# Kernel tuning notes

Hardware: AMD Instinct MI355X
Metric: run time of the kernel (lower is better)

Reference implementation:

```python
import jax, jax.numpy as jnp
import numpy as np


def _gelu(x):
    # torch F.gelu default = exact (erf) gelu
    return jax.nn.gelu(x, approximate=False)


def _gatv2(x, src, dst, Wl, bl, Wr, br, att, bout, n):
    """PyG GATv2Conv, concat=False (mean over heads), negative_slope=0.2."""
    H, C = att.shape
    xl = (x @ Wl + bl).reshape(n, H, C)  # source-side transform (messages)
    xr = (x @ Wr + br).reshape(n, H, C)  # target-side transform
    e = jax.nn.leaky_relu(xl[src] + xr[dst], 0.2)      # [E,H,C]
    logits = jnp.einsum('ehc,hc->eh', e, att)          # [E,H]
    # segment softmax over incoming edges of each target node
    m = jax.ops.segment_max(logits, dst, num_segments=n)
    m = jnp.where(jnp.isfinite(m), m, 0.0)
    p = jnp.exp(logits - m[dst])
    den = jax.ops.segment_sum(p, dst, num_segments=n)
    alpha = p / (den[dst] + 1e-16)
    out = jax.ops.segment_sum(alpha[:, :, None] * xl[src], dst, num_segments=n)  # [N,H,C]
    return out.mean(axis=1) + bout


def _gnorm(x, w, b, ms):
    """PyG GraphNorm with a single graph (batch == zeros)."""
    mu = x.mean(axis=0, keepdims=True)
    o = x - ms * mu
    var = (o * o).mean(axis=0, keepdims=True)
    return w * o / jnp.sqrt(var + 1e-5) + b


def setup_inputs() -> dict:
    N, E, HID, LAT = 50000, 300000, 128, 256
    key = jax.random.key(0)
    ks = iter(jax.random.split(key, 48))

    def rn(shape, s=0.05):
        return jax.random.normal(next(ks), shape, jnp.float32) * s

    d = {}
    d['z_g'] = rn((1, LAT), 1.0)
    d['edge_index'] = jax.random.randint(next(ks), (2, E), 0, N, dtype=jnp.int32)
    d['template_vertices'] = rn((N, 3), 1.0)
    d['W_ne1'] = rn((3, HID)); d['b_ne1'] = jnp.zeros((HID,))
    d['W_ne2'] = rn((HID, HID)); d['b_ne2'] = jnp.zeros((HID,))
    d['W_s1'] = rn((LAT, HID)); d['b_s1'] = jnp.zeros((HID,))
    d['W_s2'] = rn((HID, HID)); d['b_s2'] = jnp.zeros((HID,))
    for i, h in ((1, 2), (2, 2), (3, 1)):
        d[f'Wl{i}'] = rn((HID, h * HID)); d[f'bl{i}'] = jnp.zeros((h * HID,))
        d[f'Wr{i}'] = rn((HID, h * HID)); d[f'br{i}'] = jnp.zeros((h * HID,))
        d[f'att{i}'] = rn((h, HID)); d[f'bo{i}'] = jnp.zeros((HID,))
        d[f'gn{i}_w'] = jnp.ones((HID,)); d[f'gn{i}_b'] = jnp.zeros((HID,))
        d[f'gn{i}_ms'] = jnp.ones((HID,))
    d['W_h1'] = rn((HID, HID // 2)); d['b_h1'] = jnp.zeros((HID // 2,))
    d['W_h2'] = rn((HID // 2, 3)); d['b_h2'] = jnp.zeros((3,))
    return d


def reference(z_g, edge_index, template_vertices,
              W_ne1, b_ne1, W_ne2, b_ne2, W_s1, b_s1, W_s2, b_s2,
              Wl1, bl1, Wr1, br1, att1, bo1, gn1_w, gn1_b, gn1_ms,
              Wl2, bl2, Wr2, br2, att2, bo2, gn2_w, gn2_b, gn2_ms,
              Wl3, bl3, Wr3, br3, att3, bo3, gn3_w, gn3_b, gn3_ms,
              W_h1, b_h1, W_h2, b_h2):
    n = template_vertices.shape[0]
    sl = jnp.arange(n, dtype=edge_index.dtype)
    src = jnp.concatenate([edge_index[0], sl])  # GATv2Conv add_self_loops=True
    dst = jnp.concatenate([edge_index[1], sl])
    # node embedding + broadcast style (eval mode -> dropout is identity)
    x = _gelu(template_vertices @ W_ne1 + b_ne1) @ W_ne2 + b_ne2
    style = _gelu(z_g @ W_s1 + b_s1) @ W_s2 + b_s2   # [1, hidden]
    x = x + style
    x = _gelu(_gnorm(_gatv2(x, src, dst, Wl1, bl1, Wr1, br1, att1, bo1, n), gn1_w, gn1_b, gn1_ms))
    x = _gelu(_gnorm(_gatv2(x, src, dst, Wl2, bl2, Wr2, br2, att2, bo2, n), gn2_w, gn2_b, gn2_ms))
    x = _gelu(_gnorm(_gatv2(x, src, dst, Wl3, bl3, Wr3, br3, att3, bo3, n), gn3_w, gn3_b, gn3_ms))
    displacement = _gelu(x @ W_h1 + b_h1) @ W_h2 + b_h2   # [n, 3]
    return displacement
```

## Files before the change

### kernel.cpp

```cpp
#include <hip/hip_runtime.h>
#include <hip/hip_fp16.h>
#include <math.h>

#define DEVINL __device__ __forceinline__

using bf16x8 = __attribute__((ext_vector_type(8))) short;
using f32x4  = __attribute__((ext_vector_type(4))) float;
using u16x4  = __attribute__((ext_vector_type(4))) unsigned short;
using f16x2  = __attribute__((ext_vector_type(2))) _Float16;

DEVINL float gelu_f(float v) { return 0.5f * v * (1.0f + erff(v * 0.7071067811865475f)); }
DEVINL float lrelu_f(float v) { return v > 0.0f ? v : 0.2f * v; }
DEVINL unsigned short f2bf(float f) {
    union { float f; unsigned u; } c; c.f = f;
    unsigned r = c.u + 0x7fffu + ((c.u >> 16) & 1u);
    return (unsigned short)(r >> 16);
}
DEVINL float bf2f(unsigned short s) {
    union { unsigned u; float f; } c; c.u = (unsigned)s << 16;
    return c.f;
}
DEVINL unsigned short f2h(float f) {
    __half h = __float2half_rn(f);
    return *(unsigned short*)&h;
}
DEVINL f16x2 b2h2(unsigned u) {
    union { unsigned u; f16x2 h; } c; c.u = u; return c.h;
}
DEVINL void gl_lds16(const void* g, void* l) {
    __builtin_amdgcn_global_load_lds(
        (const __attribute__((address_space(1))) unsigned*)g,
        (__attribute__((address_space(3))) unsigned*)l, 16, 0, 0);
}

__global__ void style_k(const float* __restrict__ zg, const float* __restrict__ W1,
                        const float* __restrict__ b1, const float* __restrict__ W2,
                        const float* __restrict__ b2, float* __restrict__ style) {
    __shared__ float s1[128];
    int j = threadIdx.x;
    float a = b1[j];
    for (int k = 0; k < 256; k++) a = fmaf(zg[k], W1[k * 128 + j], a);
    s1[j] = gelu_f(a);
    __syncthreads();
    float o = b2[j];
    for (int k = 0; k < 128; k++) o = fmaf(s1[k], W2[k * 128 + j], o);
    style[j] = o;
}

__global__ void ne1_k(const float* __restrict__ tv, const float* __restrict__ W,
                      const float* __restrict__ b, float* __restrict__ h1,
                      int* __restrict__ counts, int Nn) {
    int idx = blockIdx.x * blockDim.x + threadIdx.x;
    if (idx < Nn) counts[idx] = 0;
    if (idx >= Nn * 128) return;
    int n = idx >> 7, c = idx & 127;
    float o = fmaf(tv[n * 3 + 0], W[c],
              fmaf(tv[n * 3 + 1], W[128 + c],
              fmaf(tv[n * 3 + 2], W[256 + c], b[c])));
    h1[idx] = gelu_f(o);
}

struct PrepArgs {
    const float* src[8];
    unsigned short* dst;
    int dstoff[8];
    int off[9];
    int shift[8];
};
__global__ void prep_k(PrepArgs a) {
    int idx = blockIdx.x * 256 + threadIdx.x;
    if (idx >= a.off[8]) return;
    int s = 0;
    while (idx >= a.off[s + 1]) s++;
    int e = idx - a.off[s];
    int sh = a.shift[s];
    int k = e >> sh, j = e & ((1 << sh) - 1);
    float w = a.src[s][e];
    unsigned short hi = f2bf(w);
    unsigned short lo = f2bf(w - bf2f(hi));
    int c = j >> 4, lr = j & 15;
    int s2 = k >> 5, lk = (k >> 3) & 3, i = k & 7;
    int lane = lk * 16 + lr;
    size_t base = (size_t)a.dstoff[s] + (size_t)c * 4096 + s2 * 512 + lane * 8 + i;
    a.dst[base] = hi;
    a.dst[base + 2048] = lo;
}

template <int OUT, int EPI, bool DUAL, typename OutT>
__global__ __launch_bounds__(256) void mfma_lin_k(
    const float* __restrict__ xin,
    const unsigned short* __restrict__ WT0, const float* __restrict__ b0,
    const unsigned short* __restrict__ WT1, const float* __restrict__ b1,
    const float* __restrict__ style,
    OutT* __restrict__ out0, OutT* __restrict__ out1, int Nn) {
    constexpr int CPM = OUT / 16;
    constexpr int NCH = (DUAL ? 2 : 1) * CPM;
    __shared__ uint4 buf[2][512];
    int t = threadIdx.x;
    int wave = t >> 6, lane = t & 63;
    int lr = lane & 15, lk = lane >> 4;
    int base = blockIdx.x * 128 + wave * 32;
    int r0 = base + lr, r1 = base + 16 + lr;
    int cr0 = min(r0, Nn - 1), cr1 = min(r1, Nn - 1);

    bf16x8 xh[2][4], xlo[2][4];
#pragma unroll
    for (int rr = 0; rr < 2; rr++) {
        const float* px = xin + (size_t)(rr ? cr1 : cr0) * 128;
#pragma unroll
        for (int s = 0; s < 4; s++) {
            const float4* p4 = (const float4*)(px + s * 32 + lk * 8);
            float4 a = p4[0], b = p4[1];
            float v[8] = {a.x, a.y, a.z, a.w, b.x, b.y, b.z, b.w};
            bf16x8 h, l;
#pragma unroll
            for (int i = 0; i < 8; i++) {
                unsigned short hb = f2bf(v[i]);
                h[i] = (short)hb;
                l[i] = (short)f2bf(v[i] - bf2f(hb));
            }
            xh[rr][s] = h;
            xlo[rr][s] = l;
        }
    }

    auto stage = [&](int c, int bsel) {
        const unsigned short* Wt = (DUAL && c >= CPM) ? WT1 : WT0;
        int cc = (DUAL && c >= CPM) ? c - CPM : c;
        const char* g = (const char*)(Wt + (size_t)cc * 4096);
        char* l = (char*)&buf[bsel][0];
        gl_lds16(g + t * 16, l + wave * 1024);
        gl_lds16(g + 4096 + t * 16, l + 4096 + wave * 1024);
    };

    stage(0, 0);
    for (int c = 0; c < NCH; ++c) {
        int cur = c & 1;
        bool pre = (c + 1 < NCH);
        if (pre) stage(c + 1, cur ^ 1);
        if (pre) asm volatile("s_waitcnt vmcnt(2)" ::: "memory");
        else     asm volatile("s_waitcnt vmcnt(0)" ::: "memory");
        __builtin_amdgcn_s_barrier();

        int m = (DUAL && c >= CPM) ? 1 : 0;
        int j0 = (c - m * CPM) * 16;
        const float* bias = m ? b1 : b0;
        OutT* out = m ? out1 : out0;
        const bf16x8* W = (const bf16x8*)&buf[cur][0];

        f32x4 acc0 = {0.f, 0.f, 0.f, 0.f}, acc1 = {0.f, 0.f, 0.f, 0.f};
#pragma unroll
        for (int s = 0; s < 4; ++s) {
            bf16x8 wh = W[s * 64 + lane];
            bf16x8 wl = W[256 + s * 64 + lane];
            acc0 = __builtin_amdgcn_mfma_f32_16x16x32_bf16(wh, xh[0][s], acc0, 0, 0, 0);
            acc0 = __builtin_amdgcn_mfma_f32_16x16x32_bf16(wh, xlo[0][s], acc0, 0, 0, 0);
            acc0 = __builtin_amdgcn_mfma_f32_16x16x32_bf16(wl, xh[0][s], acc0, 0, 0, 0);
            acc1 = __builtin_amdgcn_mfma_f32_16x16x32_bf16(wh, xh[1][s], acc1, 0, 0, 0);
            acc1 = __builtin_amdgcn_mfma_f32_16x16x32_bf16(wh, xlo[1][s], acc1, 0, 0, 0);
            acc1 = __builtin_amdgcn_mfma_f32_16x16x32_bf16(wl, xh[1][s], acc1, 0, 0, 0);
        }
        int j = j0 + lk * 4;
        float o0[4], o1[4];
#pragma unroll
        for (int i = 0; i < 4; i++) {
            float bb = bias[j + i];
            if (EPI == 1) bb += style[j + i];
            float v0 = acc0[i] + bb, v1 = acc1[i] + bb;
            if (EPI == 2) { v0 = gelu_f(v0); v1 = gelu_f(v1); }
            o0[i] = v0; o1[i] = v1;
        }
        if constexpr (sizeof(OutT) == 2) {
            u16x4 s0 = {f2h(o0[0]), f2h(o0[1]), f2h(o0[2]), f2h(o0[3])};
            u16x4 s1v = {f2h(o1[0]), f2h(o1[1]), f2h(o1[2]), f2h(o1[3])};
            if (r0 < Nn) *(u16x4*)((unsigned short*)out + (size_t)r0 * OUT + j) = s0;
            if (r1 < Nn) *(u16x4*)((unsigned short*)out + (size_t)r1 * OUT + j) = s1v;
        } else {
            if (r0 < Nn) { f32x4 v = {o0[0], o0[1], o0[2], o0[3]}; *(f32x4*)((float*)out + (size_t)r0 * OUT + j) = v; }
            if (r1 < Nn) { f32x4 v = {o1[0], o1[1], o1[2], o1[3]}; *(f32x4*)((float*)out + (size_t)r1 * OUT + j) = v; }
        }
        __builtin_amdgcn_s_barrier();
    }
}

__global__ void count_k(const int* __restrict__ dst, int* __restrict__ counts, int E, int EP) {
    int e = blockIdx.x * blockDim.x + threadIdx.x;
    if (e >= EP) return;
    int d = (e < E) ? dst[e] : (e - E);
    atomicAdd(&counts[d], 1);
}

__global__ void tile_sum_k(const int* __restrict__ counts, int* __restrict__ tsum, int Nn) {
    int i = blockIdx.x * 256 + threadIdx.x;
    int v = (i < Nn) ? counts[i] : 0;
    int lane = threadIdx.x & 63, wave = threadIdx.x >> 6;
#pragma unroll
    for (int off = 1; off < 64; off <<= 1) v += __shfl_xor(v, off, 64);
    __shared__ int red[4];
    if (lane == 0) red[wave] = v;
    __syncthreads();
    if (threadIdx.x == 0) tsum[blockIdx.x] = red[0] + red[1] + red[2] + red[3];
}

__global__ void tile_scan_k(const int* __restrict__ tsum, int* __restrict__ toff,
                            int ntiles, int* __restrict__ rowptr, int Nn, int total) {
    __shared__ int s[256];
    int t = threadIdx.x;
    int v = (t < ntiles) ? tsum[t] : 0;
    s[t] = v;
    __syncthreads();
    for (int off = 1; off < 256; off <<= 1) {
        int a = (t >= off) ? s[t - off] : 0;
        __syncthreads();
        s[t] += a;
        __syncthreads();
    }
    if (t < ntiles) toff[t] = s[t] - v;
    if (t == 0) rowptr[Nn] = total;
}

__global__ void tile_write_k(const int* __restrict__ counts, const int* __restrict__ toff,
                             int* __restrict__ rowptr, int* __restrict__ fillc, int Nn) {
    int i = blockIdx.x * 256 + threadIdx.x;
    int t = threadIdx.x;
    int v = (i < Nn) ? counts[i] : 0;
    if (i < Nn) fillc[i] = 0;
    __shared__ int s[256];
    s[t] = v;
    __syncthreads();
    for (int off = 1; off < 256; off <<= 1) {
        int a = (t >= off) ? s[t - off] : 0;
        __syncthreads();
        s[t] += a;
        __syncthreads();
    }
    if (i < Nn) rowptr[i] = toff[blockIdx.x] + s[t] - v;
}

__global__ void fill_k(const int* __restrict__ src, const int* __restrict__ dst,
                       const int* __restrict__ rowptr, int* __restrict__ fillc,
                       int* __restrict__ col, int E, int EP) {
    int e = blockIdx.x * blockDim.x + threadIdx.x;
    if (e >= EP) return;
    int d = (e < E) ? dst[e] : (e - E);
    int s = (e < E) ? src[e] : (e - E);
    int pos = atomicAdd(&fillc[d], 1);
    col[rowptr[d] + pos] = s;
}

template <int H>
__global__ __launch_bounds__(256) void gat_gather_k(
    const unsigned short* __restrict__ xl, const unsigned short* __restrict__ xr,
    const float* __restrict__ att, const float* __restrict__ bo,
    const int* __restrict__ rowptr, const int* __restrict__ col,
    float* __restrict__ y, float* __restrict__ stats, int Nn) {
    if (blockIdx.x == 0 && threadIdx.x < 256) stats[threadIdx.x] = 0.f;
    constexpr int NPB = (H == 2) ? 2 : 4;
    int w = threadIdx.x >> 6;
    int slot = (H == 2) ? (w >> 1) : w;
    int h = (H == 2) ? (w & 1) : 0;
    int lane = threadIdx.x & 63;
    int g = lane >> 4, sub = lane & 15;
    constexpr int HC = H * 128;
    int n = blockIdx.x * NPB + slot;
    bool act = n < Nn;
    int nn = act ? n : 0;

    uint4 uxr = *(const uint4*)(xr + (size_t)nn * HC + h * 128 + sub * 8);
    f16x2 xrv[4] = {b2h2(uxr.x), b2h2(uxr.y), b2h2(uxr.z), b2h2(uxr.w)};
    const float* ap = att + h * 128 + sub * 8;
    f16x2 a2[4];
#pragma unroll
    for (int i = 0; i < 4; i++) {
        f16x2 t; t.x = (_Float16)ap[2 * i]; t.y = (_Float16)ap[2 * i + 1];
        a2[i] = t;
    }
    f16x2 c02; c02.x = (_Float16)0.2f; c02.y = (_Float16)0.2f;

    float den = 0.f;
    float acc[8] = {0.f, 0.f, 0.f, 0.f, 0.f, 0.f, 0.f, 0.f};
    int beg = act ? rowptr[n] : 0, endp = act ? rowptr[n + 1] : 0;

    for (int k0 = beg; k0 < endp; k0 += 4) {
        int k = k0 + g;
        bool ev = k < endp;
        int s = col[ev ? k : beg];
        uint4 u = *(const uint4*)(xl + (size_t)s * HC + h * 128 + sub * 8);
        f16x2 v2[4] = {b2h2(u.x), b2h2(u.y), b2h2(u.z), b2h2(u.w)};
        float p = 0.f;
#pragma unroll
        for (int i = 0; i < 4; i++) {
            f16x2 t = v2[i] + xrv[i];
            f16x2 e = __builtin_elementwise_max(t, t * c02);
#if __has_builtin(__builtin_amdgcn_fdot2)
            p = __builtin_amdgcn_fdot2(e, a2[i], p, false);
#else
            p = fmaf((float)e.x, (float)a2[i].x, p);
            p = fmaf((float)e.y, (float)a2[i].y, p);
#endif
        }
        p += __shfl_xor(p, 1, 64);
        p += __shfl_xor(p, 2, 64);
        p += __shfl_xor(p, 4, 64);
        p += __shfl_xor(p, 8, 64);
        float pe = ev ? __expf(p) : 0.f;
        den += pe;
#pragma unroll
        for (int i = 0; i < 4; i++) {
            acc[2 * i]     = fmaf(pe, (float)v2[i].x, acc[2 * i]);
            acc[2 * i + 1] = fmaf(pe, (float)v2[i].y, acc[2 * i + 1]);
        }
    }
#pragma unroll
    for (int off = 16; off <= 32; off <<= 1) {
        den += __shfl_xor(den, off, 64);
#pragma unroll
        for (int j = 0; j < 8; j++) acc[j] += __shfl_xor(acc[j], off, 64);
    }
    float inv = 1.0f / (den + 1e-16f);

    if constexpr (H == 1) {
        if (act && g == 0) {
            const float* bp = bo + sub * 8;
            f32x4 o0 = {acc[0] * inv + bp[0], acc[1] * inv + bp[1], acc[2] * inv + bp[2], acc[3] * inv + bp[3]};
            f32x4 o1 = {acc[4] * inv + bp[4], acc[5] * inv + bp[5], acc[6] * inv + bp[6], acc[7] * inv + bp[7]};
            *(f32x4*)(y + (size_t)n * 128 + sub * 8) = o0;
            *(f32x4*)(y + (size_t)n * 128 + sub * 8 + 4) = o1;
        }
    } else {
        __shared__ float sh[NPB][2][128];
        if (g == 0) {
#pragma unroll
            for (int j = 0; j < 8; j++) sh[slot][h][sub * 8 + j] = acc[j] * inv;
        }
        __syncthreads();
        int t = threadIdx.x;
        int slot2 = t >> 7, c = t & 127;
        int n2 = blockIdx.x * NPB + slot2;
        if (n2 < Nn)
            y[(size_t)n2 * 128 + c] = (sh[slot2][0][c] + sh[slot2][1][c]) * 0.5f + bo[c];
    }
}

__global__ void gn_stats_k(const float* __restrict__ y, float* __restrict__ stats, int Nn) {
    int c = threadIdx.x;
    int per = (Nn + gridDim.x - 1) / gridDim.x;
    int n0 = blockIdx.x * per, n1 = min(n0 + per, Nn);
    float s = 0.f, s2 = 0.f;
    for (int n = n0; n < n1; n++) {
        float v = y[(size_t)n * 128 + c];
        s += v;
        s2 = fmaf(v, v, s2);
    }
    atomicAdd(&stats[c], s);
    atomicAdd(&stats[128 + c], s2);
}

__global__ void gn_apply_k(const float* __restrict__ y, const float* __restrict__ stats,
                           const float* __restrict__ w, const float* __restrict__ b,
                           const float* __restrict__ ms, float* __restrict__ xo, int Nn) {
    int i4 = blockIdx.x * blockDim.x + threadIdx.x;
    if (i4 >= Nn * 32) return;
    float4 v = reinterpret_cast<const float4*>(y)[i4];
    int c0 = (i4 & 31) * 4;
    float o[4] = {v.x, v.y, v.z, v.w};
    float invN = 1.0f / (float)Nn;
#pragma unroll
    for (int jj = 0; jj < 4; jj++) {
        int c = c0 + jj;
        float mu = stats[c] * invN;
        float ex2 = stats[128 + c] * invN;
        float msv = ms[c];
        float var = ex2 - 2.f * msv * mu * mu + msv * msv * mu * mu;
        float ov = o[jj] - msv * mu;
        float r = rsqrtf(var + 1e-5f);
        o[jj] = gelu_f(fmaf(w[c], ov * r, b[c]));
    }
    float4 res = make_float4(o[0], o[1], o[2], o[3]);
    reinterpret_cast<float4*>(xo)[i4] = res;
}

__global__ void head2_k(const float* __restrict__ h, const float* __restrict__ W,
                        const float* __restrict__ b, float* __restrict__ out, int Nn) {
    __shared__ float w[192];
    __shared__ float bb[3];
    int t = threadIdx.x;
    if (t < 192) w[t] = W[t];
    if (t < 3) bb[t] = b[t];
    __syncthreads();
    int n = blockIdx.x * blockDim.x + t;
    if (n >= Nn) return;
    float a0 = bb[0], a1 = bb[1], a2 = bb[2];
    const float4* h4 = reinterpret_cast<const float4*>(h + (size_t)n * 64);
    for (int k4 = 0; k4 < 16; k4++) {
        float4 v = h4[k4];
        int k = k4 * 4;
        a0 = fmaf(v.x, w[(k + 0) * 3 + 0], a0); a1 = fmaf(v.x, w[(k + 0) * 3 + 1], a1); a2 = fmaf(v.x, w[(k + 0) * 3 + 2], a2);
        a0 = fmaf(v.y, w[(k + 1) * 3 + 0], a0); a1 = fmaf(v.y, w[(k + 1) * 3 + 1], a1); a2 = fmaf(v.y, w[(k + 1) * 3 + 2], a2);
        a0 = fmaf(v.z, w[(k + 2) * 3 + 0], a0); a1 = fmaf(v.z, w[(k + 2) * 3 + 1], a1); a2 = fmaf(v.z, w[(k + 2) * 3 + 2], a2);
        a0 = fmaf(v.w, w[(k + 3) * 3 + 0], a0); a1 = fmaf(v.w, w[(k + 3) * 3 + 1], a1); a2 = fmaf(v.w, w[(k + 3) * 3 + 2], a2);
    }
    out[n * 3 + 0] = a0;
    out[n * 3 + 1] = a1;
    out[n * 3 + 2] = a2;
}

extern "C" void kernel_launch(void* const* d_in, const int* in_sizes, int n_in,
                              void* d_out, int out_size, void* d_ws, size_t ws_size,
                              hipStream_t stream) {
    const float* zg = (const float*)d_in[0];
    const int* ei = (const int*)d_in[1];
    const float* tv = (const float*)d_in[2];
    const float* W_ne1 = (const float*)d_in[3];
    const float* b_ne1 = (const float*)d_in[4];
    const float* W_ne2 = (const float*)d_in[5];
    const float* b_ne2 = (const float*)d_in[6];
    const float* W_s1 = (const float*)d_in[7];
    const float* b_s1 = (const float*)d_in[8];
    const float* W_s2 = (const float*)d_in[9];
    const float* b_s2 = (const float*)d_in[10];
    const float *Wl[3], *bl[3], *Wr[3], *br[3], *attp[3], *bop[3], *gnw[3], *gnb[3], *gnms[3];
    for (int L = 0; L < 3; L++) {
        int base = 11 + L * 9;
        Wl[L] = (const float*)d_in[base + 0];
        bl[L] = (const float*)d_in[base + 1];
        Wr[L] = (const float*)d_in[base + 2];
        br[L] = (const float*)d_in[base + 3];
        attp[L] = (const float*)d_in[base + 4];
        bop[L] = (const float*)d_in[base + 5];
        gnw[L] = (const float*)d_in[base + 6];
        gnb[L] = (const float*)d_in[base + 7];
        gnms[L] = (const float*)d_in[base + 8];
    }
    const float* W_h1 = (const float*)d_in[38];
    const float* b_h1 = (const float*)d_in[39];
    const float* W_h2 = (const float*)d_in[40];
    const float* b_h2 = (const float*)d_in[41];

    int E = in_sizes[1] / 2;
    int N = in_sizes[2] / 3;
    int EP = E + N;
    int NT = (N + 255) / 256;
    const int* srcp = ei;
    const int* dstp = ei + E;

    char* p = (char*)d_ws;
    auto alloc = [&](size_t bytes) -> char* {
        char* r = p;
        p += (bytes + 255) & ~(size_t)255;
        return r;
    };
    float* style = (float*)alloc(512);
    float* h1 = (float*)alloc((size_t)N * 128 * 4);
    float* x = (float*)alloc((size_t)N * 128 * 4);
    unsigned short* xle = (unsigned short*)alloc((size_t)N * 256 * 2);
    unsigned short* xre = (unsigned short*)alloc((size_t)N * 256 * 2);
    float* y = (float*)alloc((size_t)N * 128 * 4);
    float* hb = (float*)alloc((size_t)N * 64 * 4);
    float* stats = (float*)alloc(1024);
    int* rowptr = (int*)alloc(((size_t)N + 1) * 4);
    int* counts = (int*)alloc((size_t)N * 4);
    int* fillc = (int*)alloc((size_t)N * 4);
    int* col = (int*)alloc((size_t)EP * 4);
    int* tsum = (int*)alloc((size_t)NT * 4);
    int* toff = (int*)alloc((size_t)NT * 4);
    unsigned short* wt = (unsigned short*)alloc((size_t)376832 * 2);

    PrepArgs pa;
    const float* srcs[8] = {W_ne2, Wl[0], Wr[0], Wl[1], Wr[1], Wl[2], Wr[2], W_h1};
    int outs[8] = {128, 256, 256, 256, 256, 128, 128, 64};
    int off = 0;
    pa.dst = wt;
    for (int s = 0; s < 8; s++) {
        pa.src[s] = srcs[s];
        pa.off[s] = off;
        pa.dstoff[s] = 2 * off;
        pa.shift[s] = (outs[s] == 256) ? 8 : (outs[s] == 128 ? 7 : 6);
        off += 128 * outs[s];
    }
    pa.off[8] = off;
    const unsigned short* ws_ne2 = wt + pa.dstoff[0];
    const unsigned short* ws_l[3] = {wt + pa.dstoff[1], wt + pa.dstoff[3], wt + pa.dstoff[5]};
    const unsigned short* ws_r[3] = {wt + pa.dstoff[2], wt + pa.dstoff[4], wt + pa.dstoff[6]};
    const unsigned short* ws_h1 = wt + pa.dstoff[7];
    prep_k<<<(off + 255) / 256, 256, 0, stream>>>(pa);

    style_k<<<1, 128, 0, stream>>>(zg, W_s1, b_s1, W_s2, b_s2, style);
    ne1_k<<<(N * 128 + 255) / 256, 256, 0, stream>>>(tv, W_ne1, b_ne1, h1, counts, N);
    mfma_lin_k<128, 1, false, float><<<(N + 127) / 128, 256, 0, stream>>>(
        h1, ws_ne2, b_ne2, nullptr, nullptr, style, x, nullptr, N);

    count_k<<<(EP + 255) / 256, 256, 0, stream>>>(dstp, counts, E, EP);
    tile_sum_k<<<NT, 256, 0, stream>>>(counts, tsum, N);
    tile_scan_k<<<1, 256, 0, stream>>>(tsum, toff, NT, rowptr, N, EP);
    tile_write_k<<<NT, 256, 0, stream>>>(counts, toff, rowptr, fillc, N);
    fill_k<<<(EP + 255) / 256, 256, 0, stream>>>(srcp, dstp, rowptr, fillc, col, E, EP);

    const int HS[3] = {2, 2, 1};
    for (int L = 0; L < 3; L++) {
        if (HS[L] == 2) {
            mfma_lin_k<256, 0, true, unsigned short><<<(N + 127) / 128, 256, 0, stream>>>(
                x, ws_l[L], bl[L], ws_r[L], br[L], nullptr, xle, xre, N);
            gat_gather_k<2><<<(N + 1) / 2, 256, 0, stream>>>(xle, xre, attp[L], bop[L], rowptr, col, y, stats, N);
        } else {
            mfma_lin_k<128, 0, true, unsigned short><<<(N + 127) / 128, 256, 0, stream>>>(
                x, ws_l[L], bl[L], ws_r[L], br[L], nullptr, xle, xre, N);
            gat_gather_k<1><<<(N + 3) / 4, 256, 0, stream>>>(xle, xre, attp[L], bop[L], rowptr, col, y, stats, N);
        }
        gn_stats_k<<<512, 128, 0, stream>>>(y, stats, N);
        gn_apply_k<<<(N * 32 + 255) / 256, 256, 0, stream>>>(y, stats, gnw[L], gnb[L], gnms[L], x, N);
    }

    mfma_lin_k<64, 2, false, float><<<(N + 127) / 128, 256, 0, stream>>>(
        x, ws_h1, b_h1, nullptr, nullptr, nullptr, hb, nullptr, N);
    head2_k<<<(N + 255) / 256, 256, 0, stream>>>(hb, W_h2, b_h2, (float*)d_out, N);
}
```

Baseline: 667.0 us.

## Fuse GraphNorm apply and GELU into the next linear layer's input load

The full-tensor GraphNorm apply kernel is replaced by a tiny per-channel kernel that folds the mean, variance and affine parameters into a scale/shift pair (A, B). The following MFMA linear kernel reads the raw GAT output and applies gelu(A*x+B) while converting its input to bf16. This removes one full read and write of the N×128 activation per layer, plus a large launch. The cost is erf-based GELU evaluated inside the GEMM input path, and a small extra launch.

```diff
diff --git a/kernel.cpp b/kernel.cpp
--- a/kernel.cpp
+++ b/kernel.cpp
@@ -10,7 +10,6 @@
 using f16x2  = __attribute__((ext_vector_type(2))) _Float16;
 
 DEVINL float gelu_f(float v) { return 0.5f * v * (1.0f + erff(v * 0.7071067811865475f)); }
-DEVINL float lrelu_f(float v) { return v > 0.0f ? v : 0.2f * v; }
 DEVINL unsigned short f2bf(float f) {
     union { float f; unsigned u; } c; c.f = f;
     unsigned r = c.u + 0x7fffu + ((c.u >> 16) & 1u);
@@ -86,12 +85,12 @@
     a.dst[base + 2048] = lo;
 }
 
-template <int OUT, int EPI, bool DUAL, typename OutT>
+template <int OUT, int EPI, bool DUAL, typename OutT, int PRE>
 __global__ __launch_bounds__(256) void mfma_lin_k(
     const float* __restrict__ xin,
     const unsigned short* __restrict__ WT0, const float* __restrict__ b0,
     const unsigned short* __restrict__ WT1, const float* __restrict__ b1,
-    const float* __restrict__ style,
+    const float* __restrict__ style, const float* __restrict__ AB,
     OutT* __restrict__ out0, OutT* __restrict__ out1, int Nn) {
     constexpr int CPM = OUT / 16;
     constexpr int NCH = (DUAL ? 2 : 1) * CPM;
@@ -102,16 +101,29 @@
     int base = blockIdx.x * 128 + wave * 32;
     int r0 = base + lr, r1 = base + 16 + lr;
     int cr0 = min(r0, Nn - 1), cr1 = min(r1, Nn - 1);
+    const float* px0 = xin + (size_t)cr0 * 128;
+    const float* px1 = xin + (size_t)cr1 * 128;
 
     bf16x8 xh[2][4], xlo[2][4];
 #pragma unroll
-    for (int rr = 0; rr < 2; rr++) {
-        const float* px = xin + (size_t)(rr ? cr1 : cr0) * 128;
-#pragma unroll
-        for (int s = 0; s < 4; s++) {
-            const float4* p4 = (const float4*)(px + s * 32 + lk * 8);
+    for (int s = 0; s < 4; s++) {
+        int cb = s * 32 + lk * 8;
+        float A_[8], B_[8];
+        if constexpr (PRE == 2) {
+            *(f32x4*)&A_[0] = *(const f32x4*)(AB + cb);
+            *(f32x4*)&A_[4] = *(const f32x4*)(AB + cb + 4);
+            *(f32x4*)&B_[0] = *(const f32x4*)(AB + 128 + cb);
+            *(f32x4*)&B_[4] = *(const f32x4*)(AB + 128 + cb + 4);
+        }
+#pragma unroll
+        for (int rr = 0; rr < 2; rr++) {
+            const float4* p4 = (const float4*)((rr ? px1 : px0) + cb);
             float4 a = p4[0], b = p4[1];
             float v[8] = {a.x, a.y, a.z, a.w, b.x, b.y, b.z, b.w};
+            if constexpr (PRE == 2) {
+#pragma unroll
+                for (int i = 0; i < 8; i++) v[i] = gelu_f(fmaf(A_[i], v[i], B_[i]));
+            }
             bf16x8 h, l;
 #pragma unroll
             for (int i = 0; i < 8; i++) {
@@ -356,28 +368,18 @@
     atomicAdd(&stats[128 + c], s2);
 }
 
-__global__ void gn_apply_k(const float* __restrict__ y, const float* __restrict__ stats,
-                           const float* __restrict__ w, const float* __restrict__ b,
-                           const float* __restrict__ ms, float* __restrict__ xo, int Nn) {
-    int i4 = blockIdx.x * blockDim.x + threadIdx.x;
-    if (i4 >= Nn * 32) return;
-    float4 v = reinterpret_cast<const float4*>(y)[i4];
-    int c0 = (i4 & 31) * 4;
-    float o[4] = {v.x, v.y, v.z, v.w};
-    float invN = 1.0f / (float)Nn;
-#pragma unroll
-    for (int jj = 0; jj < 4; jj++) {
-        int c = c0 + jj;
-        float mu = stats[c] * invN;
-        float ex2 = stats[128 + c] * invN;
-        float msv = ms[c];
-        float var = ex2 - 2.f * msv * mu * mu + msv * msv * mu * mu;
-        float ov = o[jj] - msv * mu;
-        float r = rsqrtf(var + 1e-5f);
-        o[jj] = gelu_f(fmaf(w[c], ov * r, b[c]));
-    }
-    float4 res = make_float4(o[0], o[1], o[2], o[3]);
-    reinterpret_cast<float4*>(xo)[i4] = res;
+__global__ void gn_final_k(const float* __restrict__ stats, const float* __restrict__ w,
+                           const float* __restrict__ b, const float* __restrict__ ms,
+                           float* __restrict__ AB, float invN) {
+    int c = threadIdx.x;
+    float mu = stats[c] * invN;
+    float ex2 = stats[128 + c] * invN;
+    float msv = ms[c];
+    float var = ex2 - 2.f * msv * mu * mu + msv * msv * mu * mu;
+    float r = rsqrtf(var + 1e-5f);
+    float A = w[c] * r;
+    AB[c] = A;
+    AB[128 + c] = b[c] - A * msv * mu;
 }
 
 __global__ void head2_k(const float* __restrict__ h, const float* __restrict__ W,
@@ -458,6 +460,7 @@
     float* y = (float*)alloc((size_t)N * 128 * 4);
     float* hb = (float*)alloc((size_t)N * 64 * 4);
     float* stats = (float*)alloc(1024);
+    float* AB = (float*)alloc(1024);
     int* rowptr = (int*)alloc(((size_t)N + 1) * 4);
     int* counts = (int*)alloc((size_t)N * 4);
     int* fillc = (int*)alloc((size_t)N * 4);
@@ -485,10 +488,12 @@
     const unsigned short* ws_h1 = wt + pa.dstoff[7];
     prep_k<<<(off + 255) / 256, 256, 0, stream>>>(pa);
 
+    float invN = 1.0f / (float)N;
+
     style_k<<<1, 128, 0, stream>>>(zg, W_s1, b_s1, W_s2, b_s2, style);
     ne1_k<<<(N * 128 + 255) / 256, 256, 0, stream>>>(tv, W_ne1, b_ne1, h1, counts, N);
-    mfma_lin_k<128, 1, false, float><<<(N + 127) / 128, 256, 0, stream>>>(
-        h1, ws_ne2, b_ne2, nullptr, nullptr, style, x, nullptr, N);
+    mfma_lin_k<128, 1, false, float, 0><<<(N + 127) / 128, 256, 0, stream>>>(
+        h1, ws_ne2, b_ne2, nullptr, nullptr, style, nullptr, x, nullptr, N);
 
     count_k<<<(EP + 255) / 256, 256, 0, stream>>>(dstp, counts, E, EP);
     tile_sum_k<<<NT, 256, 0, stream>>>(counts, tsum, N);
@@ -496,22 +501,25 @@
     tile_write_k<<<NT, 256, 0, stream>>>(counts, toff, rowptr, fillc, N);
     fill_k<<<(EP + 255) / 256, 256, 0, stream>>>(srcp, dstp, rowptr, fillc, col, E, EP);
 
-    const int HS[3] = {2, 2, 1};
-    for (int L = 0; L < 3; L++) {
-        if (HS[L] == 2) {
-            mfma_lin_k<256, 0, true, unsigned short><<<(N + 127) / 128, 256, 0, stream>>>(
-                x, ws_l[L], bl[L], ws_r[L], br[L], nullptr, xle, xre, N);
-            gat_gather_k<2><<<(N + 1) / 2, 256, 0, stream>>>(xle, xre, attp[L], bop[L], rowptr, col, y, stats, N);
-        } else {
-            mfma_lin_k<128, 0, true, unsigned short><<<(N + 127) / 128, 256, 0, stream>>>(
-                x, ws_l[L], bl[L], ws_r[L], br[L], nullptr, xle, xre, N);
-            gat_gather_k<1><<<(N + 3) / 4, 256, 0, stream>>>(xle, xre, attp[L], bop[L], rowptr, col, y, stats, N);
-        }
-        gn_stats_k<<<512, 128, 0, stream>>>(y, stats, N);
-        gn_apply_k<<<(N * 32 + 255) / 256, 256, 0, stream>>>(y, stats, gnw[L], gnb[L], gnms[L], x, N);
-    }
-
-    mfma_lin_k<64, 2, false, float><<<(N + 127) / 128, 256, 0, stream>>>(
-        x, ws_h1, b_h1, nullptr, nullptr, nullptr, hb, nullptr, N);
+    mfma_lin_k<256, 0, true, unsigned short, 0><<<(N + 127) / 128, 256, 0, stream>>>(
+        x, ws_l[0], bl[0], ws_r[0], br[0], nullptr, nullptr, xle, xre, N);
+    gat_gather_k<2><<<(N + 1) / 2, 256, 0, stream>>>(xle, xre, attp[0], bop[0], rowptr, col, y, stats, N);
+    gn_stats_k<<<512, 128, 0, stream>>>(y, stats, N);
+    gn_final_k<<<1, 128, 0, stream>>>(stats, gnw[0], gnb[0], gnms[0], AB, invN);
+
+    mfma_lin_k<256, 0, true, unsigned short, 2><<<(N + 127) / 128, 256, 0, stream>>>(
+        y, ws_l[1], bl[1], ws_r[1], br[1], nullptr, AB, xle, xre, N);
+    gat_gather_k<2><<<(N + 1) / 2, 256, 0, stream>>>(xle, xre, attp[1], bop[1], rowptr, col, y, stats, N);
+    gn_stats_k<<<512, 128, 0, stream>>>(y, stats, N);
+    gn_final_k<<<1, 128, 0, stream>>>(stats, gnw[1], gnb[1], gnms[1], AB, invN);
+
+    mfma_lin_k<128, 0, true, unsigned short, 2><<<(N + 127) / 128, 256, 0, stream>>>(
+        y, ws_l[2], bl[2], ws_r[2], br[2], nullptr, AB, xle, xre, N);
+    gat_gather_k<1><<<(N + 3) / 4, 256, 0, stream>>>(xle, xre, attp[2], bop[2], rowptr, col, y, stats, N);
+    gn_stats_k<<<512, 128, 0, stream>>>(y, stats, N);
+    gn_final_k<<<1, 128, 0, stream>>>(stats, gnw[2], gnb[2], gnms[2], AB, invN);
+
+    mfma_lin_k<64, 2, false, float, 2><<<(N + 127) / 128, 256, 0, stream>>>(
+        y, ws_h1, b_h1, nullptr, nullptr, nullptr, AB, hb, nullptr, N);
     head2_k<<<(N + 255) / 256, 256, 0, stream>>>(hb, W_h2, b_h2, (float*)d_out, N);
 }
```

New measurement: 607.2 us. -9.0%, faster.
